# Kernel tuning notes

Measured on AMD Instinct MI355X. Metric: run time of the kernel, lower is better.

Reference implementation:

```python
import jax, jax.numpy as jnp
import numpy as np

N_CELLS = 50000
HID = 64
DEG = 16
K_NODES = 4  # nodes per cell; cell i owns nodes [4i, 4i+4)
SP = 3


def setup_inputs() -> dict:
    key = jax.random.key(0)
    ks = jax.random.split(key, 12)
    s = 1.0 / np.sqrt(HID)
    inp = {
        'features': jax.random.normal(ks[0], (N_CELLS, HID), jnp.float32),
        'positions': jax.random.normal(ks[1], (K_NODES * N_CELLS, SP), jnp.float32),
        'neighbors': jax.random.randint(ks[2], (N_CELLS, DEG), 0, N_CELLS, jnp.int32),
        # message MLP: Linear(2H+1 -> H), SiLU, Linear(H -> H)
        'W1': jax.random.normal(ks[3], (2 * HID + 1, HID), jnp.float32) * s,
        'b1': jnp.zeros((HID,), jnp.float32),
        'W2': jax.random.normal(ks[4], (HID, HID), jnp.float32) * s,
        'b2': jnp.zeros((HID,), jnp.float32),
        # update MLP: Linear(H + H -> H), SiLU, Linear(H -> H)
        'Wu1': jax.random.normal(ks[5], (2 * HID, HID), jnp.float32) * s,
        'bu1': jnp.zeros((HID,), jnp.float32),
        'Wu2': jax.random.normal(ks[6], (HID, HID), jnp.float32) * s,
        'bu2': jnp.zeros((HID,), jnp.float32),
    }
    return inp


def reference(features, positions, neighbors, W1, b1, W2, b2, Wu1, bu1, Wu2, bu2):
    N, H = features.shape
    # centroid of each cell's owned nodes (cell i -> nodes [K*i, K*i+K))
    cent = positions.reshape(N, K_NODES, SP).mean(axis=1)          # [N, sp]
    fj = features[neighbors]                                       # [N, D, H]
    cj = cent[neighbors]                                           # [N, D, sp]
    # centroid-distance geometric invariant per (cell, neighbor) pair
    geom = jnp.linalg.norm(cent[:, None, :] - cj, axis=-1, keepdims=True)  # [N, D, 1]
    fi = jnp.broadcast_to(features[:, None, :], fj.shape)          # [N, D, H]
    x = jnp.concatenate([fi, fj, geom], axis=-1)                   # [N, D, 2H+1]
    h = jax.nn.silu(x @ W1 + b1) @ W2 + b2                         # [N, D, H]
    msg = h.mean(axis=1)                                           # mean over neighbors
    u = jnp.concatenate([features, msg], axis=-1)                  # [N, 2H]
    upd = jax.nn.silu(u @ Wu1 + bu1) @ Wu2 + bu2
    updated_features = features + upd
    return updated_features, positions
```

## Files before the change

kernel.cpp:

```cpp
#include <hip/hip_runtime.h>


#define DEG 16

typedef __attribute__((ext_vector_type(8))) short short8;
typedef __attribute__((ext_vector_type(4))) float f32x4;
typedef uint2 uint2_a __attribute__((may_alias));
typedef uint4 uint4_a __attribute__((may_alias));

union HbRd { uint4_a u; short8 s; };
union Frag { short8 s; uint4 u; };

__device__ __forceinline__ unsigned f2bf(float f) {
  unsigned u = __float_as_uint(f);
  return (u + 0x7FFFu + ((u >> 16) & 1u)) >> 16;
}
__device__ __forceinline__ float bf2f(unsigned bits16) {
  return __uint_as_float(bits16 << 16);
}
__device__ __forceinline__ float silu(float h) {
  return h / (1.f + __expf(-h));
}

__global__ __launch_bounds__(256) void aux_kernel(
    const float* __restrict__ pos,
    const float* __restrict__ W1, const float* __restrict__ W2,
    const float* __restrict__ Wu1, const float* __restrict__ Wu2,
    float* __restrict__ outpos,
    unsigned short* __restrict__ w1pq, unsigned short* __restrict__ w2t,
    unsigned short* __restrict__ wu1t, unsigned short* __restrict__ wu2b)
{
  int t = blockIdx.x * 256 + threadIdx.x;
  if (t < 150000) {
    ((float4*)outpos)[t] = ((const float4*)pos)[t];
  } else if (t < 174576) {
    const int r = t - 150000;
    if (r < 8192) {
      const int j = r & 7, l = (r >> 3) & 15, q = (r >> 7) & 3;
      const int f = r >> 9, kk = f & 1, mt = f >> 1;
      const int k = kk * 32 + q * 8 + j;
      const int m = mt * 16 + l;
      w1pq[r] = (unsigned short)f2bf(
          (m < 64) ? W1[k * 64 + m] : W1[(k + 64) * 64 + (m - 64)]);
    } else if (r < 12288) {
      const int s = r - 8192;
      const int j = s & 7, l = (s >> 3) & 15, q = (s >> 7) & 3;
      const int f = s >> 9, kk = f & 1, mt = f >> 1;
      const int k = kk * 32 + q * 8 + j;
      w2t[s] = (unsigned short)f2bf(W2[k * 64 + mt * 16 + l]);
    } else if (r < 20480) {
      const int s = r - 12288;
      const int j = s & 7, l = (s >> 3) & 15, q = (s >> 7) & 3;
      const int f = s >> 9, kk = f & 3, mt = f >> 2;
      const int k = kk * 32 + q * 8 + j;
      wu1t[s] = (unsigned short)f2bf(Wu1[k * 64 + mt * 16 + l]);
    } else {
      const int s = r - 20480;
      const int j = s & 7, l = (s >> 3) & 15, q = (s >> 7) & 3;
      const int f = s >> 9, kk = f & 1, nt = f >> 1;
      const int k = kk * 32 + q * 8 + j;
      wu2b[s] = (unsigned short)f2bf(Wu2[k * 64 + nt * 16 + l]);
    }
  }
}

__global__ __launch_bounds__(256) void prep_pq_kernel(
    const float* __restrict__ feat, const float* __restrict__ pos,
    const unsigned short* __restrict__ w1pq,
    unsigned short* __restrict__ featb, float* __restrict__ cent4,
    unsigned short* __restrict__ Pb, unsigned short* __restrict__ Qb)
{
  const int lane = threadIdx.x & 63;
  const int wid  = threadIdx.x >> 6;
  const int quad = lane >> 4;
  const int l15  = lane & 15;

  const int tile = blockIdx.x * 4 + wid;
  const bool act = (tile < 3125);
  const int  tt  = act ? tile : 3124;
  const int  cr  = tt * 16 + l15;

  short8 xf[2];
  #pragma unroll
  for (int kk = 0; kk < 2; ++kk) {
    const float4 f0 = *(const float4*)(feat + cr * 64 + kk * 32 + quad * 8);
    const float4 f1 = *(const float4*)(feat + cr * 64 + kk * 32 + quad * 8 + 4);
    Frag v;
    v.s[0] = (short)f2bf(f0.x); v.s[1] = (short)f2bf(f0.y);
    v.s[2] = (short)f2bf(f0.z); v.s[3] = (short)f2bf(f0.w);
    v.s[4] = (short)f2bf(f1.x); v.s[5] = (short)f2bf(f1.y);
    v.s[6] = (short)f2bf(f1.z); v.s[7] = (short)f2bf(f1.w);
    xf[kk] = v.s;
    if (act) *(uint4*)(featb + cr * 64 + kk * 32 + quad * 8) = v.u;
  }

  if (act && lane < 16) {
    const float4* pp = (const float4*)(pos + 12 * cr);
    const float4 a = pp[0], b = pp[1], c = pp[2];
    float4 o;
    o.x = (a.x + a.w + b.z + c.y) * 0.25f;
    o.y = (a.y + b.x + b.w + c.z) * 0.25f;
    o.z = (a.z + b.y + c.x + c.w) * 0.25f;
    o.w = 0.f;
    ((float4*)cent4)[cr] = o;
  }

  short8 wf[8][2];
  #pragma unroll
  for (int mt = 0; mt < 8; ++mt)
    #pragma unroll
    for (int kk = 0; kk < 2; ++kk)
      wf[mt][kk] = *(const short8*)(w1pq + (((mt * 2 + kk) * 4 + quad) << 7) + l15 * 8);

  f32x4 acc[8] = {};
  #pragma unroll
  for (int kk = 0; kk < 2; ++kk)
    #pragma unroll
    for (int mt = 0; mt < 8; ++mt)
      acc[mt] = __builtin_amdgcn_mfma_f32_16x16x32_bf16(wf[mt][kk], xf[kk], acc[mt], 0, 0, 0);

  if (act) {
    #pragma unroll
    for (int mt = 0; mt < 8; ++mt) {
      uint2 pk;
      pk.x = f2bf(acc[mt][0]) | (f2bf(acc[mt][1]) << 16);
      pk.y = f2bf(acc[mt][2]) | (f2bf(acc[mt][3]) << 16);
      unsigned short* dst = (mt < 4)
          ? Pb + cr * 64 + mt * 16 + quad * 4
          : Qb + cr * 64 + (mt - 4) * 16 + quad * 4;
      *(uint2*)dst = pk;
    }
  }
}

__global__ __launch_bounds__(256) void gather_kernel(
    const unsigned short* __restrict__ Pb,
    const unsigned short* __restrict__ Qb,
    const float4* __restrict__ cent4,
    const int* __restrict__ nbr,
    const float* __restrict__ b1, const float* __restrict__ W1,
    unsigned short* __restrict__ sB)
{
  const int lane = threadIdx.x & 63;
  const int wid  = threadIdx.x >> 6;
  const int c    = blockIdx.x * 4 + wid;

  const int nj = nbr[c * DEG + (lane & 15)];

  const float4 ci = cent4[c];
  const float4 cj = cent4[nj];
  const float dx = ci.x - cj.x, dy = ci.y - cj.y, dz = ci.z - cj.z;
  const float g = sqrtf(dx * dx + dy * dy + dz * dz);

  const float pcb = bf2f(Pb[c * 64 + lane]) + b1[lane];
  const float wl  = W1[8192 + lane];

  float acc = 0.f;
  #pragma unroll
  for (int d = 0; d < DEG; ++d) {
    const int   nd = __builtin_amdgcn_readlane(nj, d);
    const float gd = __uint_as_float(
        __builtin_amdgcn_readlane((int)__float_as_uint(g), d));
    const float qv = bf2f(Qb[nd * 64 + lane]);
    acc += silu(pcb + qv + gd * wl);
  }

  sB[c * 64 + lane] = (unsigned short)f2bf(acc * 0.0625f);
}

__global__ __launch_bounds__(256) void tail_kernel(
    const unsigned short* __restrict__ featb,
    const unsigned short* __restrict__ sB,
    const float* __restrict__ feat,
    const unsigned short* __restrict__ w2t,
    const unsigned short* __restrict__ wu1t,
    const unsigned short* __restrict__ wu2b,
    const float* __restrict__ b2, const float* __restrict__ bu1,
    const float* __restrict__ bu2,
    float* __restrict__ outf)
{
  __shared__ uint4 smem[4 * 288];
  const int lane = threadIdx.x & 63;
  const int wid  = threadIdx.x >> 6;
  const int quad = lane >> 4;
  const int l15  = lane & 15;
  char* Msg = (char*)(smem + wid * 288);
  char* Hb  = Msg + 2304;

  short8 w2f[4][2];
  #pragma unroll
  for (int mt = 0; mt < 4; ++mt)
    #pragma unroll
    for (int kk = 0; kk < 2; ++kk)
      w2f[mt][kk] = *(const short8*)(w2t + (((mt * 2 + kk) * 4 + quad) << 7) + l15 * 8);
  short8 wu1f[4][4];
  #pragma unroll
  for (int mt = 0; mt < 4; ++mt)
    #pragma unroll
    for (int kk = 0; kk < 4; ++kk)
      wu1f[mt][kk] = *(const short8*)(wu1t + (((mt * 4 + kk) * 4 + quad) << 7) + l15 * 8);
  short8 wu2f[4][2];
  #pragma unroll
  for (int nt = 0; nt < 4; ++nt)
    #pragma unroll
    for (int kk = 0; kk < 2; ++kk)
      wu2f[nt][kk] = *(const short8*)(wu2b + (((nt * 2 + kk) * 4 + quad) << 7) + l15 * 8);

  f32x4 b2f[4], bu1f[4];
  #pragma unroll
  for (int mt = 0; mt < 4; ++mt) {
    b2f[mt]  = *(const f32x4*)(b2  + mt * 16 + quad * 4);
    bu1f[mt] = *(const f32x4*)(bu1 + mt * 16 + quad * 4);
  }
  float bu2v[4];
  #pragma unroll
  for (int nt = 0; nt < 4; ++nt) bu2v[nt] = bu2[nt * 16 + l15];

  const int tile = blockIdx.x * 4 + wid;
  const bool act = (tile < 3125);
  const int  tt  = act ? tile : 3124;
  const int  cr  = tt * 16 + l15;

  f32x4 accm[4] = {};
  #pragma unroll
  for (int kk = 0; kk < 2; ++kk) {
    const short8 bf = *(const short8*)(sB + cr * 64 + kk * 32 + quad * 8);
    #pragma unroll
    for (int mt = 0; mt < 4; ++mt)
      accm[mt] = __builtin_amdgcn_mfma_f32_16x16x32_bf16(w2f[mt][kk], bf, accm[mt], 0, 0, 0);
  }
  #pragma unroll
  for (int mt = 0; mt < 4; ++mt) {
    uint2 pk;
    pk.x = f2bf(accm[mt][0] + b2f[mt][0]) | (f2bf(accm[mt][1] + b2f[mt][1]) << 16);
    pk.y = f2bf(accm[mt][2] + b2f[mt][2]) | (f2bf(accm[mt][3] + b2f[mt][3]) << 16);
    *(uint2_a*)(Msg + l15 * 144 + mt * 32 + quad * 8) = pk;
  }
  __threadfence_block();

  f32x4 accu[4] = {};
  #pragma unroll
  for (int kk = 0; kk < 4; ++kk) {
    short8 bf;
    if (kk < 2) {
      bf = *(const short8*)(featb + cr * 64 + kk * 32 + quad * 8);
    } else {
      HbRd t; t.u = *(const uint4_a*)(Msg + l15 * 144 + (kk - 2) * 64 + quad * 16);
      bf = t.s;
    }
    #pragma unroll
    for (int mt = 0; mt < 4; ++mt)
      accu[mt] = __builtin_amdgcn_mfma_f32_16x16x32_bf16(wu1f[mt][kk], bf, accu[mt], 0, 0, 0);
  }
  #pragma unroll
  for (int mt = 0; mt < 4; ++mt) {
    float sv[4];
    #pragma unroll
    for (int rg = 0; rg < 4; ++rg)
      sv[rg] = silu(accu[mt][rg] + bu1f[mt][rg]);
    uint2 pk;
    pk.x = f2bf(sv[0]) | (f2bf(sv[1]) << 16);
    pk.y = f2bf(sv[2]) | (f2bf(sv[3]) << 16);
    *(uint2_a*)(Hb + l15 * 144 + mt * 32 + quad * 8) = pk;
  }
  __threadfence_block();

  f32x4 acc2[4] = {};
  #pragma unroll
  for (int kk = 0; kk < 2; ++kk) {
    HbRd t; t.u = *(const uint4_a*)(Hb + l15 * 144 + kk * 64 + quad * 16);
    const short8 af = t.s;
    #pragma unroll
    for (int nt = 0; nt < 4; ++nt)
      acc2[nt] = __builtin_amdgcn_mfma_f32_16x16x32_bf16(af, wu2f[nt][kk], acc2[nt], 0, 0, 0);
  }
  if (act) {
    #pragma unroll
    for (int nt = 0; nt < 4; ++nt)
      #pragma unroll
      for (int rg = 0; rg < 4; ++rg) {
        const int row = tt * 16 + quad * 4 + rg;
        const int col = nt * 16 + l15;
        outf[row * 64 + col] = feat[row * 64 + col] + acc2[nt][rg] + bu2v[nt];
      }
  }
}

extern "C" void kernel_launch(void* const* d_in, const int* in_sizes, int n_in,
                              void* d_out, int out_size, void* d_ws, size_t ws_size,
                              hipStream_t stream)
{
  const float* feat = (const float*)d_in[0];
  const float* pos  = (const float*)d_in[1];
  const int*   nbr  = (const int*)d_in[2];
  const float* W1   = (const float*)d_in[3];
  const float* b1   = (const float*)d_in[4];
  const float* W2   = (const float*)d_in[5];
  const float* b2   = (const float*)d_in[6];
  const float* Wu1  = (const float*)d_in[7];
  const float* bu1  = (const float*)d_in[8];
  const float* Wu2  = (const float*)d_in[9];
  const float* bu2  = (const float*)d_in[10];
  float* out = (float*)d_out;

  unsigned short* featb = (unsigned short*)d_ws;
  unsigned short* Pb    = (unsigned short*)((char*)d_ws + 6400000);
  unsigned short* Qb    = (unsigned short*)((char*)d_ws + 12800000);
  unsigned short* sB    = (unsigned short*)((char*)d_ws + 19200000);
  float*          cent4 = (float*)((char*)d_ws + 25600000);
  unsigned short* w1pq  = (unsigned short*)((char*)d_ws + 26400000);
  unsigned short* w2t   = (unsigned short*)((char*)d_ws + 26416384);
  unsigned short* wu1t  = (unsigned short*)((char*)d_ws + 26424576);
  unsigned short* wu2b  = (unsigned short*)((char*)d_ws + 26440960);

  aux_kernel<<<682, 256, 0, stream>>>(pos, W1, W2, Wu1, Wu2, out + 3200000,
                                      w1pq, w2t, wu1t, wu2b);
  prep_pq_kernel<<<782, 256, 0, stream>>>(feat, pos, w1pq, featb, cent4, Pb, Qb);
  gather_kernel<<<12500, 256, 0, stream>>>(Pb, Qb, (const float4*)cent4, nbr,
                                           b1, W1, sB);
  tail_kernel<<<782, 256, 0, stream>>>(featb, sB, feat, w2t, wu1t, wu2b,
                                       b2, bu1, bu2, out);
}
```

Before: 141.4 us.

## Split Q table into column halves and gather each half in a separate pass

```diff
diff --git a/kernel.cpp b/kernel.cpp
--- a/kernel.cpp
+++ b/kernel.cpp
@@ -68,7 +68,8 @@
     const float* __restrict__ feat, const float* __restrict__ pos,
     const unsigned short* __restrict__ w1pq,
     unsigned short* __restrict__ featb, float* __restrict__ cent4,
-    unsigned short* __restrict__ Pb, unsigned short* __restrict__ Qb)
+    unsigned short* __restrict__ Pb,
+    unsigned short* __restrict__ Q0, unsigned short* __restrict__ Q1)
 {
   const int lane = threadIdx.x & 63;
   const int wid  = threadIdx.x >> 6;
@@ -125,25 +126,29 @@
       uint2 pk;
       pk.x = f2bf(acc[mt][0]) | (f2bf(acc[mt][1]) << 16);
       pk.y = f2bf(acc[mt][2]) | (f2bf(acc[mt][3]) << 16);
-      unsigned short* dst = (mt < 4)
-          ? Pb + cr * 64 + mt * 16 + quad * 4
-          : Qb + cr * 64 + (mt - 4) * 16 + quad * 4;
+      unsigned short* dst;
+      if (mt < 4)      dst = Pb + cr * 64 + mt * 16 + quad * 4;
+      else if (mt < 6) dst = Q0 + cr * 32 + (mt - 4) * 16 + quad * 4;
+      else             dst = Q1 + cr * 32 + (mt - 6) * 16 + quad * 4;
       *(uint2*)dst = pk;
     }
   }
 }
 
-__global__ __launch_bounds__(256) void gather_kernel(
+__global__ __launch_bounds__(256) void gather_half_kernel(
+    const unsigned short* __restrict__ Qh,
     const unsigned short* __restrict__ Pb,
-    const unsigned short* __restrict__ Qb,
     const float4* __restrict__ cent4,
     const int* __restrict__ nbr,
     const float* __restrict__ b1, const float* __restrict__ W1,
-    unsigned short* __restrict__ sB)
+    unsigned short* __restrict__ sB,
+    int colofs)
 {
   const int lane = threadIdx.x & 63;
   const int wid  = threadIdx.x >> 6;
-  const int c    = blockIdx.x * 4 + wid;
+  const int sub  = lane >> 5;
+  const int col  = lane & 31;
+  const int c    = (blockIdx.x * 4 + wid) * 2 + sub;
 
   const int nj = nbr[c * DEG + (lane & 15)];
 
@@ -152,20 +157,25 @@
   const float dx = ci.x - cj.x, dy = ci.y - cj.y, dz = ci.z - cj.z;
   const float g = sqrtf(dx * dx + dy * dy + dz * dz);
 
-  const float pcb = bf2f(Pb[c * 64 + lane]) + b1[lane];
-  const float wl  = W1[8192 + lane];
+  const float pcb = bf2f(Pb[c * 64 + colofs + col]) + b1[colofs + col];
+  const float wl  = W1[8192 + colofs + col];
 
   float acc = 0.f;
   #pragma unroll
   for (int d = 0; d < DEG; ++d) {
-    const int   nd = __builtin_amdgcn_readlane(nj, d);
-    const float gd = __uint_as_float(
+    const int   n0 = __builtin_amdgcn_readlane(nj, d);
+    const int   n1 = __builtin_amdgcn_readlane(nj, 32 + d);
+    const float g0 = __uint_as_float(
         __builtin_amdgcn_readlane((int)__float_as_uint(g), d));
-    const float qv = bf2f(Qb[nd * 64 + lane]);
-    acc += silu(pcb + qv + gd * wl);
-  }
-
-  sB[c * 64 + lane] = (unsigned short)f2bf(acc * 0.0625f);
+    const float g1 = __uint_as_float(
+        __builtin_amdgcn_readlane((int)__float_as_uint(g), 32 + d));
+    const int   ndl = sub ? n1 : n0;
+    const float gdl = sub ? g1 : g0;
+    const float qv  = bf2f(Qh[ndl * 32 + col]);
+    acc += silu(pcb + qv + gdl * wl);
+  }
+
+  sB[c * 64 + colofs + col] = (unsigned short)f2bf(acc * 0.0625f);
 }
 
 __global__ __launch_bounds__(256) void tail_kernel(
@@ -305,7 +315,8 @@
 
   unsigned short* featb = (unsigned short*)d_ws;
   unsigned short* Pb    = (unsigned short*)((char*)d_ws + 6400000);
-  unsigned short* Qb    = (unsigned short*)((char*)d_ws + 12800000);
+  unsigned short* Q0    = (unsigned short*)((char*)d_ws + 12800000);
+  unsigned short* Q1    = (unsigned short*)((char*)d_ws + 16000000);
   unsigned short* sB    = (unsigned short*)((char*)d_ws + 19200000);
   float*          cent4 = (float*)((char*)d_ws + 25600000);
   unsigned short* w1pq  = (unsigned short*)((char*)d_ws + 26400000);
@@ -315,9 +326,12 @@
 
   aux_kernel<<<682, 256, 0, stream>>>(pos, W1, W2, Wu1, Wu2, out + 3200000,
                                       w1pq, w2t, wu1t, wu2b);
-  prep_pq_kernel<<<782, 256, 0, stream>>>(feat, pos, w1pq, featb, cent4, Pb, Qb);
-  gather_kernel<<<12500, 256, 0, stream>>>(Pb, Qb, (const float4*)cent4, nbr,
-                                           b1, W1, sB);
+  prep_pq_kernel<<<782, 256, 0, stream>>>(feat, pos, w1pq, featb, cent4,
+                                          Pb, Q0, Q1);
+  gather_half_kernel<<<6250, 256, 0, stream>>>(Q0, Pb, (const float4*)cent4,
+                                               nbr, b1, W1, sB, 0);
+  gather_half_kernel<<<6250, 256, 0, stream>>>(Q1, Pb, (const float4*)cent4,
+                                               nbr, b1, W1, sB, 32);
   tail_kernel<<<782, 256, 0, stream>>>(featb, sB, feat, w2t, wu1t, wu2b,
                                        b2, bu1, bu2, out);
 }
```

Result: slower. 155.7 us (+10.1%).
